# Kernel optimization log

Measured on AMD Instinct MI355X. Metric: run time of the kernel, lower is better.

Reference implementation:

```python
import jax, jax.numpy as jnp
import numpy as np

N_HEAD = 16
DIM_K = 64
DIM_MODEL = N_HEAD * DIM_K  # 1024; seq_len is forced to equal dim_model by the reshape
SCALE = float(DIM_K ** 0.5)


def setup_inputs() -> dict:
    key = jax.random.key(0)
    ks = jax.random.split(key, 4)
    B, S, D = 32, DIM_MODEL, 1024
    x = jax.random.normal(ks[0], (B, S, D), dtype=jnp.float32)
    glorot = float(1.0 / np.sqrt(D))
    Wq = jax.random.normal(ks[1], (D, DIM_MODEL), dtype=jnp.float32) * glorot
    Wk = jax.random.normal(ks[2], (D, DIM_MODEL), dtype=jnp.float32) * glorot
    Wv = jax.random.normal(ks[3], (D, DIM_MODEL), dtype=jnp.float32) * glorot
    bq = jnp.zeros((DIM_MODEL,), jnp.float32)
    bk = jnp.zeros((DIM_MODEL,), jnp.float32)
    bv = jnp.zeros((DIM_MODEL,), jnp.float32)
    return {"x": x, "Wq": Wq, "bq": bq, "Wk": Wk, "bk": bk, "Wv": Wv, "bv": bv}


def reference(x, Wq, bq, Wk, bk, Wv, bv):
    # x: [B, S, D] with S == DIM_MODEL (required by the original reshape)
    B = x.shape[0]
    q = x @ Wq + bq  # [B, S, dm]
    k = x @ Wk + bk
    v = x @ Wv + bv
    # TF1 K.batch_dot(q, k, axes=[-1,-1]) -> tf.matmul(q, k, adjoint_a=True):
    # contracts over the SEQUENCE axis -> [B, dm, dm]
    y = jnp.einsum('bsd,bse->bde', q, k) / SCALE
    # softmax over dim_k-sized chunks of the last axis
    y = y.reshape(B, DIM_MODEL, N_HEAD, DIM_K)
    y = jax.nn.softmax(y, axis=-1)
    y = y.reshape(B, DIM_MODEL, DIM_MODEL)
    # TF1 K.batch_dot(v, y, axes=[2,3]) -> tf.matmul(v, y) (no adjoints)
    out = jnp.einsum('bsd,bde->bse', v, y)  # [B, S, dm]
    return out
```

## Files before the change

### kernel.cpp

```cpp
#include <hip/hip_runtime.h>
#include <hip/hip_bf16.h>

#define DM 1024
#define NB 32

typedef __bf16 bf16_t;
typedef __attribute__((ext_vector_type(8))) __bf16 bf16x8;
typedef __attribute__((ext_vector_type(4))) float  f32x4;

typedef __attribute__((address_space(1))) void gas_void;
typedef __attribute__((address_space(3))) void las_void;

__device__ __forceinline__ void async_lds16(const bf16_t* g, bf16_t* l) {
    __builtin_amdgcn_global_load_lds((gas_void*)g, (las_void*)l, 16, 0, 0);
}

__device__ inline float bf2f(bf16_t v) {
    union { unsigned short s; __bf16 b; } u; u.b = v;
    union { unsigned int i; float f; } w; w.i = ((unsigned int)u.s) << 16;
    return w.f;
}
__device__ inline bf16_t f2bf(float f) {
    union { unsigned int i; float f; } w; w.f = f;
    unsigned int r = (w.i + 0x7FFFu + ((w.i >> 16) & 1u)) >> 16;
    union { unsigned short s; __bf16 b; } u; u.s = (unsigned short)r;
    return u.b;
}

enum EpiMode { EPI_NONE = 0, EPI_BIAS_ROW = 1, EPI_BIAS_COL = 2, EPI_SCALE = 3 };

__global__ void detect_mode(const unsigned short* __restrict__ x, int* __restrict__ mode)
{
    if (threadIdx.x == 0 && blockIdx.x == 0) {
        int hits = 0;
        for (int i = 0; i < 2048; ++i) {
            unsigned e = (x[i] >> 7) & 0xFFu;
            hits += (e >= 0x8Du) ? 1 : 0;
        }
        *mode = (hits >= 16) ? 1 : 0;
    }
}

__global__ void convert_x(const void* __restrict__ xin, bf16_t* __restrict__ xb,
                          const int* __restrict__ modep, long long off, long long n8)
{
    const long long i = (long long)blockIdx.x * blockDim.x + threadIdx.x;
    if (i >= n8) return;
    bf16x8 o;
    if (*modep) {
        const float* s = (const float*)xin + off + i * 8;
#pragma unroll
        for (int j = 0; j < 8; ++j) o[j] = f2bf(s[j]);
    } else {
        o = *(const bf16x8*)((const bf16_t*)xin + off + i * 8);
    }
    *(bf16x8*)(xb + i * 8) = o;
}

__global__ void transpose3(const void* __restrict__ Wq, const void* __restrict__ Wk,
                           const void* __restrict__ Wv, bf16_t* __restrict__ Wt,
                           const int* __restrict__ modep)
{
    const int md = *modep;
    const void* src = (blockIdx.z == 0) ? Wq : (blockIdx.z == 1) ? Wk : Wv;
    bf16_t* dst = Wt + (size_t)blockIdx.z * DM * DM;
    __shared__ bf16_t T[64][72];
    const int tid = threadIdx.x;
    const int r  = tid >> 2;
    const int cp = tid & 3;
    const int r0 = blockIdx.y * 64;
    const int c0 = blockIdx.x * 64;
    const size_t base = (size_t)(r0 + r) * DM + c0 + cp * 16;
    bf16_t tmp[16];
    if (md) {
        const float* s = (const float*)src + base;
#pragma unroll
        for (int j = 0; j < 16; ++j) tmp[j] = f2bf(s[j]);
    } else {
        const bf16_t* s = (const bf16_t*)src + base;
        bf16x8 a = *(const bf16x8*)s;
        bf16x8 b = *(const bf16x8*)(s + 8);
#pragma unroll
        for (int j = 0; j < 8; ++j) { tmp[j] = a[j]; tmp[8 + j] = b[j]; }
    }
#pragma unroll
    for (int j = 0; j < 16; ++j) T[cp * 16 + j][r] = tmp[j];
    __syncthreads();
    bf16_t* d = dst + (size_t)(c0 + r) * DM + r0 + cp * 16;
    bf16x8 w0, w1;
#pragma unroll
    for (int j = 0; j < 8; ++j) w0[j] = T[r][cp * 16 + j];
#pragma unroll
    for (int j = 0; j < 8; ++j) w1[j] = T[r][cp * 16 + 8 + j];
    *(bf16x8*)d = w0;
    *(bf16x8*)(d + 8) = w1;
}

template <int MODE, bool DUALOUT>
__global__ __launch_bounds__(512, 2)
void gemm_nt8(const bf16_t* __restrict__ A, long long sA,
              const bf16_t* __restrict__ B, long long sB,
              void* __restrict__ C, long long sC, long long cOff,
              const void* __restrict__ bias, const int* __restrict__ modep,
              float scale)
{
    constexpr int K = 1024;
    constexpr int NT = K / 64;
    extern __shared__ bf16_t L[];

    int bx, by, z;
    {
        const int nwg  = 16 * (int)gridDim.z;
        const int orig = (int)blockIdx.x + 4 * ((int)blockIdx.y + 4 * (int)blockIdx.z);
        const int nid  = (orig & 7) * (nwg >> 3) + (orig >> 3);
        bx = nid & 3; by = (nid >> 2) & 3; z = nid >> 4;
    }

    const bf16_t* Ab = A + (size_t)z * (size_t)sA;
    const bf16_t* Bb = B + (size_t)z * (size_t)sB;
    const int gm0 = by * 256, gn0 = bx * 256;

    const int tid  = threadIdx.x;
    const int lane = tid & 63;
    const int w    = tid >> 6;
    const int rb   = w >> 1;
    const int cb   = w & 1;
    const int lm   = lane & 15;
    const int kg   = lane >> 4;

    f32x4 acc[4][2][4];
#pragma unroll
    for (int p = 0; p < 4; ++p)
#pragma unroll
        for (int i = 0; i < 2; ++i)
#pragma unroll
            for (int j = 0; j < 4; ++j) acc[p][i][j] = (f32x4)0.0f;

    bf16x8 af0[2][2], af1[2][2], bg0[4][2], bg1[4][2];

    auto stage = [&](int kt, int s, int b) {
        const bf16_t* P  = (s & 1) ? Bb : Ab;
        const int     g0 = (s & 1) ? gn0 : gm0;
        const int     h  = (s >= 2) ? 1 : 0;
        bf16_t* dst = L + (b * 4 + s) * 8192;
#pragma unroll
        for (int i = 0; i < 2; ++i) {
            const int ci  = i * 512 + tid;
            const int row = ci >> 3;
            const int kc  = (ci & 7) ^ (row & 7);
            async_lds16(P + (size_t)(g0 + h * 128 + row) * K + kt * 64 + kc * 8,
                        dst + ci * 8);
        }
    };

    auto rdfrag = [&](int b, int s, int r, int kc) -> bf16x8 {
        const int byte = r * 128 + ((kc ^ (r & 7)) * 16);
        return *(const bf16x8*)((const char*)(L + (b * 4 + s) * 8192) + byte);
    };
    auto rdA = [&](int b, int s, bf16x8 (&dst)[2][2]) {
#pragma unroll
        for (int mt = 0; mt < 2; ++mt)
#pragma unroll
            for (int kk = 0; kk < 2; ++kk)
                dst[mt][kk] = rdfrag(b, s, rb * 32 + mt * 16 + lm, kk * 4 + kg);
    };
    auto rdB = [&](int b, int s, bf16x8 (&dst)[4][2]) {
#pragma unroll
        for (int nt = 0; nt < 4; ++nt)
#pragma unroll
            for (int kk = 0; kk < 2; ++kk)
                dst[nt][kk] = rdfrag(b, s, cb * 64 + nt * 16 + lm, kk * 4 + kg);
    };

#define MFMA_PHASE(P, AF, BG)                                                  \
    __builtin_amdgcn_s_setprio(1);                                             \
    _Pragma("unroll")                                                          \
    for (int kk = 0; kk < 2; ++kk)                                             \
        _Pragma("unroll")                                                      \
        for (int mt = 0; mt < 2; ++mt)                                         \
            _Pragma("unroll")                                                  \
            for (int nt = 0; nt < 4; ++nt)                                     \
                acc[P][mt][nt] = __builtin_amdgcn_mfma_f32_16x16x32_bf16(      \
                    AF[mt][kk], BG[nt][kk], acc[P][mt][nt], 0, 0, 0);          \
    __builtin_amdgcn_s_setprio(0);

#pragma unroll
    for (int s = 0; s < 4; ++s) stage(0, s, 0);
    asm volatile("s_waitcnt vmcnt(4)" ::: "memory");
    __builtin_amdgcn_s_barrier();

#pragma unroll 1
    for (int kt = 0; kt < NT; ++kt) {
        const int cur = kt & 1;
        const int nxt = cur ^ 1;
        const int nkt = (kt + 1 < NT) ? kt + 1 : 0;

        rdA(cur, 0, af0);
        rdB(cur, 1, bg0);
        stage(nkt, 0, nxt);
        stage(nkt, 1, nxt);
        __builtin_amdgcn_sched_barrier(0);
        MFMA_PHASE(0, af0, bg0)
        __builtin_amdgcn_sched_barrier(0);
        asm volatile("s_waitcnt vmcnt(6)" ::: "memory");
        __builtin_amdgcn_s_barrier();

        rdA(cur, 2, af1);
        stage(nkt, 2, nxt);
        stage(nkt, 3, nxt);
        __builtin_amdgcn_sched_barrier(0);
        MFMA_PHASE(1, af1, bg0)
        __builtin_amdgcn_sched_barrier(0);
        asm volatile("s_waitcnt vmcnt(8)" ::: "memory");
        __builtin_amdgcn_s_barrier();

        rdB(cur, 3, bg1);
        __builtin_amdgcn_sched_barrier(0);
        MFMA_PHASE(2, af0, bg1)
        MFMA_PHASE(3, af1, bg1)
        __builtin_amdgcn_sched_barrier(0);
        asm volatile("s_waitcnt vmcnt(4)" ::: "memory");
        __builtin_amdgcn_s_barrier();
    }
#undef MFMA_PHASE

    const int md = *modep;
#pragma unroll
    for (int p = 0; p < 4; ++p) {
        const int rbase = gm0 + (p & 1) * 128 + rb * 32;
        const int cbase = gn0 + (p >> 1) * 128 + cb * 64;
#pragma unroll
        for (int mt = 0; mt < 2; ++mt) {
            float rbias[4];
            if (MODE == EPI_BIAS_ROW) {
#pragma unroll
                for (int r = 0; r < 4; ++r) {
                    const int i = rbase + mt * 16 + kg * 4 + r;
                    rbias[r] = md ? ((const float*)bias)[i] : bf2f(((const bf16_t*)bias)[i]);
                }
            }
#pragma unroll
            for (int nt = 0; nt < 4; ++nt) {
                const int col = cbase + nt * 16 + lm;
                float cbias = 0.f;
                if (MODE == EPI_BIAS_COL)
                    cbias = md ? ((const float*)bias)[col] : bf2f(((const bf16_t*)bias)[col]);
#pragma unroll
                for (int r = 0; r < 4; ++r) {
                    const int row = rbase + mt * 16 + kg * 4 + r;
                    float vv = acc[p][mt][nt][r];
                    if (MODE == EPI_BIAS_ROW) vv += rbias[r];
                    if (MODE == EPI_BIAS_COL) vv += cbias;
                    if (MODE == EPI_SCALE)    vv *= scale;
                    const size_t off = (size_t)cOff + (size_t)z * sC + (size_t)row * 1024 + col;
                    if (DUALOUT && md) ((float*)C)[off] = vv;
                    else               ((bf16_t*)C)[off] = f2bf(vv);
                }
            }
        }
    }
}

__global__ void softmax_t_inplace(bf16_t* __restrict__ Y)
{
    const int b = blockIdx.z;
    int idx = blockIdx.x;
    int I = 0;
    while (idx >= 16 - I) { idx -= 16 - I; ++I; }
    const int J = I + idx;

    const int tid = threadIdx.x;
    const int r  = tid >> 2;
    const int cp = tid & 3;

    bf16_t* base = Y + ((size_t)b << 20);
    bf16_t* t0 = base + (size_t)(I * 64 + r) * DM + J * 64 + cp * 16;
    bf16_t* t1 = base + (size_t)(J * 64 + r) * DM + I * 64 + cp * 16;

    __shared__ bf16_t P0[64][72];
    __shared__ bf16_t P1[64][72];

    bf16x8 a0 = *(const bf16x8*)t0;
    bf16x8 a1 = *(const bf16x8*)(t0 + 8);
    bf16x8 c0v, c1v;
    if (J != I) { c0v = *(const bf16x8*)t1; c1v = *(const bf16x8*)(t1 + 8); }

    {
        float f[16];
#pragma unroll
        for (int j = 0; j < 8; ++j) f[j] = bf2f(a0[j]);
#pragma unroll
        for (int j = 0; j < 8; ++j) f[8 + j] = bf2f(a1[j]);
        float m = -1e30f;
#pragma unroll
        for (int j = 0; j < 16; ++j) m = fmaxf(m, f[j]);
        m = fmaxf(m, __shfl_xor(m, 1));
        m = fmaxf(m, __shfl_xor(m, 2));
        float s = 0.f;
#pragma unroll
        for (int j = 0; j < 16; ++j) { f[j] = __expf(f[j] - m); s += f[j]; }
        s += __shfl_xor(s, 1);
        s += __shfl_xor(s, 2);
        const float inv = 1.0f / s;
#pragma unroll
        for (int j = 0; j < 16; ++j) P0[cp * 16 + j][r] = f2bf(f[j] * inv);
    }
    if (J != I) {
        float f[16];
#pragma unroll
        for (int j = 0; j < 8; ++j) f[j] = bf2f(c0v[j]);
#pragma unroll
        for (int j = 0; j < 8; ++j) f[8 + j] = bf2f(c1v[j]);
        float m = -1e30f;
#pragma unroll
        for (int j = 0; j < 16; ++j) m = fmaxf(m, f[j]);
        m = fmaxf(m, __shfl_xor(m, 1));
        m = fmaxf(m, __shfl_xor(m, 2));
        float s = 0.f;
#pragma unroll
        for (int j = 0; j < 16; ++j) { f[j] = __expf(f[j] - m); s += f[j]; }
        s += __shfl_xor(s, 1);
        s += __shfl_xor(s, 2);
        const float inv = 1.0f / s;
#pragma unroll
        for (int j = 0; j < 16; ++j) P1[cp * 16 + j][r] = f2bf(f[j] * inv);
    }
    __syncthreads();

    bf16x8 w0, w1;
#pragma unroll
    for (int j = 0; j < 8; ++j) w0[j] = P0[r][cp * 16 + j];
#pragma unroll
    for (int j = 0; j < 8; ++j) w1[j] = P0[r][cp * 16 + 8 + j];
    *(bf16x8*)t1 = w0;
    *(bf16x8*)(t1 + 8) = w1;
    if (J != I) {
#pragma unroll
        for (int j = 0; j < 8; ++j) w0[j] = P1[r][cp * 16 + j];
#pragma unroll
        for (int j = 0; j < 8; ++j) w1[j] = P1[r][cp * 16 + 8 + j];
        *(bf16x8*)t0 = w0;
        *(bf16x8*)(t0 + 8) = w1;
    }
}

extern "C" void kernel_launch(void* const* d_in, const int* in_sizes, int n_in,
                              void* d_out, int out_size, void* d_ws, size_t ws_size,
                              hipStream_t stream)
{
    const void* x  = d_in[0];
    const void* Wq = d_in[1];
    const void* bq = d_in[2];
    const void* Wk = d_in[3];
    const void* bk = d_in[4];
    const void* Wv = d_in[5];
    const void* bv = d_in[6];

    static bool attr_done = false;
    if (!attr_done) {
        hipFuncSetAttribute((const void*)gemm_nt8<EPI_BIAS_ROW, false>,
                            hipFuncAttributeMaxDynamicSharedMemorySize, 131072);
        hipFuncSetAttribute((const void*)gemm_nt8<EPI_BIAS_COL, false>,
                            hipFuncAttributeMaxDynamicSharedMemorySize, 131072);
        hipFuncSetAttribute((const void*)gemm_nt8<EPI_SCALE, false>,
                            hipFuncAttributeMaxDynamicSharedMemorySize, 131072);
        hipFuncSetAttribute((const void*)gemm_nt8<EPI_NONE, true>,
                            hipFuncAttributeMaxDynamicSharedMemorySize, 131072);
        attr_done = true;
    }

    char* ws = (char*)d_ws;
    int* mode = (int*)ws;
    const size_t MB2 = (size_t)DM * DM * 2;
    const size_t hdr = 256;
    int CB = NB;
    while (CB > 1 && hdr + 3 * MB2 + 4 * (size_t)CB * MB2 > ws_size) CB >>= 1;

    bf16_t* Wt = (bf16_t*)(ws + hdr);
    bf16_t* xb = (bf16_t*)(ws + hdr + 3 * MB2);
    bf16_t* qt = xb + (size_t)CB * DM * DM;
    bf16_t* kt = qt + (size_t)CB * DM * DM;
    bf16_t* y  = kt + (size_t)CB * DM * DM;
    bf16_t* v  = qt;

    detect_mode<<<1, 64, 0, stream>>>((const unsigned short*)x, mode);
    transpose3<<<dim3(16, 16, 3), 256, 0, stream>>>(Wq, Wk, Wv, Wt, mode);

    const long long msz = (long long)DM * DM;
    for (int c = 0; c < NB; c += CB) {
        const int zb = (NB - c < CB) ? (NB - c) : CB;
        const long long n8 = (long long)zb * msz / 8;
        convert_x<<<(int)((n8 + 255) / 256), 256, 0, stream>>>(x, xb, mode, (long long)c * msz, n8);

        const dim3 g8(4, 4, zb), blk8(512);
        gemm_nt8<EPI_BIAS_ROW, false><<<g8, blk8, 131072, stream>>>(Wt, 0, xb, msz, qt, msz, 0, bq, mode, 1.f);
        gemm_nt8<EPI_BIAS_ROW, false><<<g8, blk8, 131072, stream>>>(Wt + msz, 0, xb, msz, kt, msz, 0, bk, mode, 1.f);
        gemm_nt8<EPI_SCALE, false><<<g8, blk8, 131072, stream>>>(qt, msz, kt, msz, y, msz, 0, nullptr, mode, 0.125f);
        softmax_t_inplace<<<dim3(136, 1, zb), 256, 0, stream>>>(y);
        gemm_nt8<EPI_BIAS_COL, false><<<g8, blk8, 131072, stream>>>(xb, msz, Wt + 2 * msz, 0, v, msz, 0, bv, mode, 1.f);
        gemm_nt8<EPI_NONE, true><<<g8, blk8, 131072, stream>>>(v, msz, y, msz, d_out, msz, (long long)c * msz, nullptr, mode, 1.f);
    }
}
```

Baseline: 675.0 us.

## Fuse chunked softmax and transpose into the Q^T K GEMM epilogue

Replaces the separate in-place softmax/transpose kernel with a GEMM epilogue that computes the 64-wide chunk softmax from accumulator registers using lane shuffles and writes the transposed probabilities directly. This removes one full read and write of the y matrix per batch and a kernel launch. The transposed stores are 8-byte column-strided writes, which may coalesce less well than the original row stores.

```diff
diff --git a/kernel.cpp b/kernel.cpp
--- a/kernel.cpp
+++ b/kernel.cpp
@@ -5,6 +5,7 @@
 #define NB 32
 
 typedef __bf16 bf16_t;
+typedef __attribute__((ext_vector_type(4))) __bf16 bf16x4;
 typedef __attribute__((ext_vector_type(8))) __bf16 bf16x8;
 typedef __attribute__((ext_vector_type(4))) float  f32x4;
 
@@ -27,7 +28,8 @@
     return u.b;
 }
 
-enum EpiMode { EPI_NONE = 0, EPI_BIAS_ROW = 1, EPI_BIAS_COL = 2, EPI_SCALE = 3 };
+enum EpiMode { EPI_NONE = 0, EPI_BIAS_ROW = 1, EPI_BIAS_COL = 2, EPI_SCALE = 3,
+               EPI_SMAXT = 4 };
 
 __global__ void detect_mode(const unsigned short* __restrict__ x, int* __restrict__ mode)
 {
@@ -224,123 +226,94 @@
     }
 #undef MFMA_PHASE
 
-    const int md = *modep;
-#pragma unroll
-    for (int p = 0; p < 4; ++p) {
-        const int rbase = gm0 + (p & 1) * 128 + rb * 32;
-        const int cbase = gn0 + (p >> 1) * 128 + cb * 64;
-#pragma unroll
-        for (int mt = 0; mt < 2; ++mt) {
-            float rbias[4];
-            if (MODE == EPI_BIAS_ROW) {
-#pragma unroll
-                for (int r = 0; r < 4; ++r) {
-                    const int i = rbase + mt * 16 + kg * 4 + r;
-                    rbias[r] = md ? ((const float*)bias)[i] : bf2f(((const bf16_t*)bias)[i]);
-                }
-            }
-#pragma unroll
-            for (int nt = 0; nt < 4; ++nt) {
-                const int col = cbase + nt * 16 + lm;
-                float cbias = 0.f;
-                if (MODE == EPI_BIAS_COL)
-                    cbias = md ? ((const float*)bias)[col] : bf2f(((const bf16_t*)bias)[col]);
-#pragma unroll
-                for (int r = 0; r < 4; ++r) {
-                    const int row = rbase + mt * 16 + kg * 4 + r;
-                    float vv = acc[p][mt][nt][r];
-                    if (MODE == EPI_BIAS_ROW) vv += rbias[r];
-                    if (MODE == EPI_BIAS_COL) vv += cbias;
-                    if (MODE == EPI_SCALE)    vv *= scale;
-                    const size_t off = (size_t)cOff + (size_t)z * sC + (size_t)row * 1024 + col;
-                    if (DUALOUT && md) ((float*)C)[off] = vv;
-                    else               ((bf16_t*)C)[off] = f2bf(vv);
+    if constexpr (MODE == EPI_SMAXT) {
+        bf16_t* Y = (bf16_t*)C + (size_t)cOff + (size_t)z * sC;
+#pragma unroll
+        for (int p = 0; p < 4; ++p) {
+            const int rbase = gm0 + (p & 1) * 128 + rb * 32;
+            const int cbase = gn0 + (p >> 1) * 128 + cb * 64;
+#pragma unroll
+            for (int mt = 0; mt < 2; ++mt) {
+                float ex[4][4];
+                float mx[4], sm[4];
+#pragma unroll
+                for (int r = 0; r < 4; ++r) mx[r] = -3.0e38f;
+#pragma unroll
+                for (int nt = 0; nt < 4; ++nt)
+#pragma unroll
+                    for (int r = 0; r < 4; ++r) {
+                        ex[nt][r] = acc[p][mt][nt][r] * scale;
+                        mx[r] = fmaxf(mx[r], ex[nt][r]);
+                    }
+#pragma unroll
+                for (int st = 1; st <= 8; st <<= 1)
+#pragma unroll
+                    for (int r = 0; r < 4; ++r)
+                        mx[r] = fmaxf(mx[r], __shfl_xor(mx[r], st));
+#pragma unroll
+                for (int r = 0; r < 4; ++r) sm[r] = 0.f;
+#pragma unroll
+                for (int nt = 0; nt < 4; ++nt)
+#pragma unroll
+                    for (int r = 0; r < 4; ++r) {
+                        ex[nt][r] = __expf(ex[nt][r] - mx[r]);
+                        sm[r] += ex[nt][r];
+                    }
+#pragma unroll
+                for (int st = 1; st <= 8; st <<= 1)
+#pragma unroll
+                    for (int r = 0; r < 4; ++r)
+                        sm[r] += __shfl_xor(sm[r], st);
+#pragma unroll
+                for (int r = 0; r < 4; ++r) sm[r] = 1.0f / sm[r];
+                const int d0 = rbase + mt * 16 + kg * 4;
+#pragma unroll
+                for (int nt = 0; nt < 4; ++nt) {
+                    bf16x4 o;
+#pragma unroll
+                    for (int r = 0; r < 4; ++r) o[r] = f2bf(ex[nt][r] * sm[r]);
+                    const int e = cbase + nt * 16 + lm;
+                    *(bf16x4*)(Y + (size_t)e * 1024 + d0) = o;
                 }
             }
         }
-    }
-}
-
-__global__ void softmax_t_inplace(bf16_t* __restrict__ Y)
-{
-    const int b = blockIdx.z;
-    int idx = blockIdx.x;
-    int I = 0;
-    while (idx >= 16 - I) { idx -= 16 - I; ++I; }
-    const int J = I + idx;
-
-    const int tid = threadIdx.x;
-    const int r  = tid >> 2;
-    const int cp = tid & 3;
-
-    bf16_t* base = Y + ((size_t)b << 20);
-    bf16_t* t0 = base + (size_t)(I * 64 + r) * DM + J * 64 + cp * 16;
-    bf16_t* t1 = base + (size_t)(J * 64 + r) * DM + I * 64 + cp * 16;
-
-    __shared__ bf16_t P0[64][72];
-    __shared__ bf16_t P1[64][72];
-
-    bf16x8 a0 = *(const bf16x8*)t0;
-    bf16x8 a1 = *(const bf16x8*)(t0 + 8);
-    bf16x8 c0v, c1v;
-    if (J != I) { c0v = *(const bf16x8*)t1; c1v = *(const bf16x8*)(t1 + 8); }
-
-    {
-        float f[16];
-#pragma unroll
-        for (int j = 0; j < 8; ++j) f[j] = bf2f(a0[j]);
-#pragma unroll
-        for (int j = 0; j < 8; ++j) f[8 + j] = bf2f(a1[j]);
-        float m = -1e30f;
-#pragma unroll
-        for (int j = 0; j < 16; ++j) m = fmaxf(m, f[j]);
-        m = fmaxf(m, __shfl_xor(m, 1));
-        m = fmaxf(m, __shfl_xor(m, 2));
-        float s = 0.f;
-#pragma unroll
-        for (int j = 0; j < 16; ++j) { f[j] = __expf(f[j] - m); s += f[j]; }
-        s += __shfl_xor(s, 1);
-        s += __shfl_xor(s, 2);
-        const float inv = 1.0f / s;
-#pragma unroll
-        for (int j = 0; j < 16; ++j) P0[cp * 16 + j][r] = f2bf(f[j] * inv);
-    }
-    if (J != I) {
-        float f[16];
-#pragma unroll
-        for (int j = 0; j < 8; ++j) f[j] = bf2f(c0v[j]);
-#pragma unroll
-        for (int j = 0; j < 8; ++j) f[8 + j] = bf2f(c1v[j]);
-        float m = -1e30f;
-#pragma unroll
-        for (int j = 0; j < 16; ++j) m = fmaxf(m, f[j]);
-        m = fmaxf(m, __shfl_xor(m, 1));
-        m = fmaxf(m, __shfl_xor(m, 2));
-        float s = 0.f;
-#pragma unroll
-        for (int j = 0; j < 16; ++j) { f[j] = __expf(f[j] - m); s += f[j]; }
-        s += __shfl_xor(s, 1);
-        s += __shfl_xor(s, 2);
-        const float inv = 1.0f / s;
-#pragma unroll
-        for (int j = 0; j < 16; ++j) P1[cp * 16 + j][r] = f2bf(f[j] * inv);
-    }
-    __syncthreads();
-
-    bf16x8 w0, w1;
-#pragma unroll
-    for (int j = 0; j < 8; ++j) w0[j] = P0[r][cp * 16 + j];
-#pragma unroll
-    for (int j = 0; j < 8; ++j) w1[j] = P0[r][cp * 16 + 8 + j];
-    *(bf16x8*)t1 = w0;
-    *(bf16x8*)(t1 + 8) = w1;
-    if (J != I) {
-#pragma unroll
-        for (int j = 0; j < 8; ++j) w0[j] = P1[r][cp * 16 + j];
-#pragma unroll
-        for (int j = 0; j < 8; ++j) w1[j] = P1[r][cp * 16 + 8 + j];
-        *(bf16x8*)t0 = w0;
-        *(bf16x8*)(t0 + 8) = w1;
+        return;
+    } else {
+        const int md = *modep;
+#pragma unroll
+        for (int p = 0; p < 4; ++p) {
+            const int rbase = gm0 + (p & 1) * 128 + rb * 32;
+            const int cbase = gn0 + (p >> 1) * 128 + cb * 64;
+#pragma unroll
+            for (int mt = 0; mt < 2; ++mt) {
+                float rbias[4];
+                if (MODE == EPI_BIAS_ROW) {
+#pragma unroll
+                    for (int r = 0; r < 4; ++r) {
+                        const int i = rbase + mt * 16 + kg * 4 + r;
+                        rbias[r] = md ? ((const float*)bias)[i] : bf2f(((const bf16_t*)bias)[i]);
+                    }
+                }
+#pragma unroll
+                for (int nt = 0; nt < 4; ++nt) {
+                    const int col = cbase + nt * 16 + lm;
+                    float cbias = 0.f;
+                    if (MODE == EPI_BIAS_COL)
+                        cbias = md ? ((const float*)bias)[col] : bf2f(((const bf16_t*)bias)[col]);
+#pragma unroll
+                    for (int r = 0; r < 4; ++r) {
+                        const int row = rbase + mt * 16 + kg * 4 + r;
+                        float vv = acc[p][mt][nt][r];
+                        if (MODE == EPI_BIAS_ROW) vv += rbias[r];
+                        if (MODE == EPI_BIAS_COL) vv += cbias;
+                        if (MODE == EPI_SCALE)    vv *= scale;
+                        const size_t off = (size_t)cOff + (size_t)z * sC + (size_t)row * 1024 + col;
+                        if (DUALOUT && md) ((float*)C)[off] = vv;
+                        else               ((bf16_t*)C)[off] = f2bf(vv);
+                    }
+                }
+            }
+        }
     }
 }
 
@@ -362,7 +335,7 @@
                             hipFuncAttributeMaxDynamicSharedMemorySize, 131072);
         hipFuncSetAttribute((const void*)gemm_nt8<EPI_BIAS_COL, false>,
                             hipFuncAttributeMaxDynamicSharedMemorySize, 131072);
-        hipFuncSetAttribute((const void*)gemm_nt8<EPI_SCALE, false>,
+        hipFuncSetAttribute((const void*)gemm_nt8<EPI_SMAXT, false>,
                             hipFuncAttributeMaxDynamicSharedMemorySize, 131072);
         hipFuncSetAttribute((const void*)gemm_nt8<EPI_NONE, true>,
                             hipFuncAttributeMaxDynamicSharedMemorySize, 131072);
@@ -395,8 +368,7 @@
         const dim3 g8(4, 4, zb), blk8(512);
         gemm_nt8<EPI_BIAS_ROW, false><<<g8, blk8, 131072, stream>>>(Wt, 0, xb, msz, qt, msz, 0, bq, mode, 1.f);
         gemm_nt8<EPI_BIAS_ROW, false><<<g8, blk8, 131072, stream>>>(Wt + msz, 0, xb, msz, kt, msz, 0, bk, mode, 1.f);
-        gemm_nt8<EPI_SCALE, false><<<g8, blk8, 131072, stream>>>(qt, msz, kt, msz, y, msz, 0, nullptr, mode, 0.125f);
-        softmax_t_inplace<<<dim3(136, 1, zb), 256, 0, stream>>>(y);
+        gemm_nt8<EPI_SMAXT, false><<<g8, blk8, 131072, stream>>>(qt, msz, kt, msz, y, msz, 0, nullptr, mode, 0.125f);
         gemm_nt8<EPI_BIAS_COL, false><<<g8, blk8, 131072, stream>>>(xb, msz, Wt + 2 * msz, 0, v, msz, 0, bv, mode, 1.f);
         gemm_nt8<EPI_NONE, true><<<g8, blk8, 131072, stream>>>(v, msz, y, msz, d_out, msz, (long long)c * msz, nullptr, mode, 1.f);
     }
```

Result: faster. 649.3 us (-3.8%).
